# Kernel optimization log

Hardware: AMD Instinct MI355X
Metric: run time of the kernel (lower is better)

## Reference

```python
import jax, jax.numpy as jnp
import numpy as np

NB, NA, NC, NH, NW = 16, 5, 80, 64, 64
MAXT = 50            # max gt boxes per image
THRESH = 0.6         # ignore threshold
NOOBJ_SCALE = 1.0
OBJ_SCALE = 5.0
NTOT = NB * NA * NH * NW


def _iou_cwh(b1, b2):
    """IoU for center-format (x,y,w,h) boxes, broadcasting over leading dims."""
    x1, y1, w1, h1 = (b1[..., i] for i in range(4))
    x2, y2, w2, h2 = (b2[..., i] for i in range(4))
    cw = jnp.minimum(x1 + 0.5 * w1, x2 + 0.5 * w2) - jnp.maximum(x1 - 0.5 * w1, x2 - 0.5 * w2)
    ch = jnp.minimum(y1 + 0.5 * h1, y2 + 0.5 * h2) - jnp.maximum(y1 - 0.5 * h1, y2 - 0.5 * h2)
    inter = jnp.maximum(cw, 0.0) * jnp.maximum(ch, 0.0)
    union = w1 * h1 + w2 * h2 - inter
    return jnp.where(inter > 0, inter / union, 0.0)


def setup_inputs() -> dict:
    key = jax.random.key(0)
    k1, k2, k3, k4 = jax.random.split(key, 4)
    output = jax.random.normal(k1, (NB, NA * (5 + NC), NH, NW), jnp.float32)
    nval = 20  # valid boxes per image; rest zero (loop-break semantics)
    cls = jax.random.randint(k2, (NB, nval), 0, NC).astype(jnp.float32)
    xy = jax.random.uniform(k3, (NB, nval, 2), minval=0.05, maxval=0.95)
    wh = jax.random.uniform(k4, (NB, nval, 2), minval=0.05, maxval=0.30)
    boxes = jnp.concatenate([cls[..., None], xy, wh], axis=-1)      # [NB,nval,5]
    pad = jnp.zeros((NB, MAXT - nval, 5), jnp.float32)
    target = jnp.concatenate([boxes, pad], axis=1).reshape(NB, MAXT * 5)
    anchors = jnp.array([[0.57273, 0.677385], [1.87446, 2.06253], [3.33843, 5.47434],
                         [7.88282, 3.52778], [9.77052, 9.16828]], jnp.float32)
    return {"output": output, "target": target, "anchors": anchors}


def reference(output, target, anchors):
    target = jax.lax.stop_gradient(target)  # target.detach() in torch
    out = output.reshape(NB, NA, 5 + NC, NH, NW)
    tx = jax.nn.sigmoid(out[:, :, 0])
    ty = jax.nn.sigmoid(out[:, :, 1])
    tw, th = out[:, :, 2], out[:, :, 3]
    conf = jax.nn.sigmoid(out[:, :, 4])                   # [B,A,H,W]
    cls_logits = jnp.moveaxis(out[:, :, 5:], 2, -1)       # [B,A,H,W,C]

    aw, ah = anchors[:, 0], anchors[:, 1]
    # decoded pred boxes, detached (only used for target building, as in torch)
    pred = jax.lax.stop_gradient(jnp.stack([
        tx + jnp.arange(NW, dtype=jnp.float32)[None, None, None, :],
        ty + jnp.arange(NH, dtype=jnp.float32)[None, None, :, None],
        jnp.exp(tw) * aw[None, :, None, None],
        jnp.exp(th) * ah[None, :, None, None]], axis=-1))  # [B,A,H,W,4]
    anchors_sg = jax.lax.stop_gradient(anchors)
    aw_sg, ah_sg = anchors_sg[:, 0], anchors_sg[:, 1]

    tb = target.reshape(NB, MAXT, 5)
    # torch breaks at first box with x==0 -> cumulative validity
    valid = jnp.cumprod((tb[:, :, 1] != 0).astype(jnp.int32), axis=1) > 0  # [B,T]
    gcls = tb[:, :, 0]
    gx, gw = tb[:, :, 1] * NW, tb[:, :, 3] * NW
    gy, gh = tb[:, :, 2] * NH, tb[:, :, 4] * NH
    gt = jnp.stack([gx, gy, gw, gh], axis=-1)             # [B,T,4]

    # ignore mask: max IoU of each pred box against all valid gt
    ious = _iou_cwh(gt[:, :, None, None, None, :], pred[:, None])  # [B,T,A,H,W]
    ious = jnp.where(valid[:, :, None, None, None], ious, 0.0)
    conf_mask = jnp.where(ious.max(axis=1) > THRESH, 0.0, NOOBJ_SCALE)  # [B,A,H,W]

    # anchor assignment: IoU of (0,0,gw,gh) vs (0,0,aw,ah) -> argmax anchor
    inter = jnp.minimum(gw[..., None], aw_sg) * jnp.minimum(gh[..., None], ah_sg)
    union = gw[..., None] * gh[..., None] + aw_sg * ah_sg - inter
    best_n = jnp.argmax(inter / union, axis=-1)           # [B,T]

    gi = jnp.clip(gx.astype(jnp.int32), 0, NW - 1)
    gj = jnp.clip(gy.astype(jnp.int32), 0, NH - 1)
    cell = best_n * (NH * NW) + gj * NW + gi              # [B,T] index in A*H*W
    mpred = jnp.take_along_axis(pred.reshape(NB, NA * NH * NW, 4), cell[:, :, None], axis=1)
    iou_best = _iou_cwh(gt, mpred)                        # [B,T]

    flat = cell + jnp.arange(NB)[:, None] * (NA * NH * NW)
    flat = jnp.where(valid, flat, NTOT).reshape(-1)       # out-of-range -> dropped
    fv = lambda v: v.reshape(-1)
    gw_s = jnp.where(valid, gw, 1.0)
    gh_s = jnp.where(valid, gh, 1.0)
    awb, ahb = aw_sg[best_n], ah_sg[best_n]

    cls_mask = jnp.zeros(NTOT, jnp.float32).at[flat].set(1.0, mode='drop')
    conf_mask = conf_mask.reshape(-1).at[flat].set(OBJ_SCALE, mode='drop')
    # seen < 12800 -> tcoord xy default 0.5, coord_mask all ones
    t0 = jnp.full((NTOT,), 0.5).at[flat].set(fv(gx - gi.astype(jnp.float32)), mode='drop')
    t1 = jnp.full((NTOT,), 0.5).at[flat].set(fv(gy - gj.astype(jnp.float32)), mode='drop')
    t2 = jnp.zeros(NTOT).at[flat].set(fv(jnp.log(gw_s / awb)), mode='drop')
    t3 = jnp.zeros(NTOT).at[flat].set(fv(jnp.log(gh_s / ahb)), mode='drop')
    tconf = jnp.zeros(NTOT).at[flat].set(fv(iou_best), mode='drop')
    tcls = jnp.zeros(NTOT, jnp.int32).at[flat].set(fv(gcls.astype(jnp.int32)), mode='drop')

    coord = jnp.stack([tx, ty, tw, th], axis=0).reshape(4, NTOT)
    tcoord = jnp.stack([t0, t1, t2, t3], axis=0)
    loss_coord = 0.5 * jnp.sum((coord - tcoord) ** 2)     # coord_mask == 1 everywhere
    loss_conf = 0.5 * jnp.sum(conf_mask * (conf.reshape(-1) - tconf) ** 2)
    logp = jax.nn.log_softmax(cls_logits, axis=-1).reshape(NTOT, NC)
    ce = -jnp.take_along_axis(logp, tcls[:, None], axis=1)[:, 0]
    loss_cls = jnp.sum(ce * cls_mask)
    return loss_coord + loss_conf + loss_cls
```

## Files before the change

### kernel.cpp

```cpp
#include <hip/hip_runtime.h>
#include <math.h>

constexpr int kNB   = 16;
constexpr int kNA   = 5;
constexpr int kNC   = 80;
constexpr int kNH   = 64;
constexpr int kNW   = 64;
constexpr int kMAXT = 50;
constexpr int kCH    = 5 + kNC;
constexpr int kPLANE = kNH * kNW;
constexpr int kCELLS_B = kNA * kPLANE;
constexpr int kBLK  = 1024;
constexpr int kBPB  = kCELLS_B / kBLK;
constexpr int kGRID = kNB * kBPB;
constexpr float kOBJ = 5.0f;
constexpr unsigned kREADY = 0x9E3779B9u;

constexpr int kRECF = 16;
constexpr int kRECB = kMAXT * kRECF;

__device__ __forceinline__ float frcp(float x) { return __builtin_amdgcn_rcpf(x); }
__device__ __forceinline__ float fsig(float x) { return frcp(1.0f + __expf(-x)); }

__global__ __launch_bounds__(64) void k_targets(const float* __restrict__ out,
                                                const float* __restrict__ target,
                                                const float* __restrict__ anchors,
                                                float* __restrict__ recG,
                                                int* __restrict__ nvArr) {
    const int b = blockIdx.x, t = threadIdx.x;

    float c0 = 0.f, x = 0.f, y = 0.f, w = 0.f, h = 0.f;
    if (t < kMAXT) {
        const float* tp = target + (b * kMAXT + t) * 5;
        c0 = tp[0]; x = tp[1]; y = tp[2]; w = tp[3]; h = tp[4];
    }
    unsigned long long m = __ballot(x != 0.0f);
    int nv = (int)__builtin_ctzll(~m);
    if (t == 0) nvArr[b] = nv;

    const bool act = (t < nv);
    int cell = -1, gi = 0, gj = 0, bn = 0;
    float gx = 0, gy = 0, gw = 0, gh = 0, aw = 1.f, ah = 1.f;
    if (act) {
        gx = x * kNW; gy = y * kNH; gw = w * kNW; gh = h * kNH;
        float best = -1.0f;
        for (int n = 0; n < kNA; ++n) {
            float aw_ = anchors[2 * n], ah_ = anchors[2 * n + 1];
            float inter = fminf(gw, aw_) * fminf(gh, ah_);
            float uni = gw * gh + aw_ * ah_ - inter;
            float r = inter / uni;
            if (r > best) { best = r; bn = n; }
        }
        aw = anchors[2 * bn]; ah = anchors[2 * bn + 1];
        gi = (int)gx; gi = gi < 0 ? 0 : (gi > kNW - 1 ? kNW - 1 : gi);
        gj = (int)gy; gj = gj < 0 ? 0 : (gj > kNH - 1 ? kNH - 1 : gj);
        cell = bn * kPLANE + gj * kNW + gi;
    }
    bool owner = act;
    for (int t2 = 0; t2 < kMAXT; ++t2) {
        int c2 = __shfl(cell, t2, 64);
        if (act && t2 > t && c2 == cell) owner = false;
    }
    if (act) {
        const float* mb = out + ((size_t)(b * kNA + bn) * kCH) * kPLANE + gj * kNW + gi;
        float px = fsig(mb[0]) + (float)gi;
        float py = fsig(mb[kPLANE]) + (float)gj;
        float pw = __expf(mb[2 * kPLANE]) * aw;
        float ph = __expf(mb[3 * kPLANE]) * ah;
        float cw  = fminf(gx + 0.5f * gw, px + 0.5f * pw) - fmaxf(gx - 0.5f * gw, px - 0.5f * pw);
        float chh = fminf(gy + 0.5f * gh, py + 0.5f * ph) - fmaxf(gy - 0.5f * gh, py - 0.5f * ph);
        float inter = fmaxf(cw, 0.f) * fmaxf(chh, 0.f);
        float uni = gw * gh + pw * ph - inter;
        float iou = (inter > 0.f) ? inter / uni : 0.f;

        float* r = recG + b * kRECB + t * kRECF;
        r[0]  = gx - 0.5f * gw;  r[1]  = gx + 0.5f * gw;
        r[2]  = gy - 0.5f * gh;  r[3]  = gy + 0.5f * gh;
        r[4]  = 0.6f * gw * gh;  r[5]  = __int_as_float(cell);
        r[6]  = owner ? 1.f : 0.f; r[7] = 0.f;
        r[8]  = gx - (float)gi;  r[9]  = gy - (float)gj;
        r[10] = __logf(gw / aw); r[11] = __logf(gh / ah);
        r[12] = iou;             r[13] = c0;
        r[14] = 0.f;             r[15] = 0.f;
    }
}

__global__ __launch_bounds__(1024) void k_fused(const float* __restrict__ out,
                                                const float* __restrict__ anchors,
                                                const float* __restrict__ recG,
                                                const int* __restrict__ nvArr,
                                                float* __restrict__ partials,
                                                unsigned* __restrict__ flags,
                                                float* __restrict__ outv) {
    __shared__ __align__(16) float srec[kRECB];
    __shared__ float wred[16];

    const int tid  = threadIdx.x;
    const int wave = tid >> 6;
    const int lane = tid & 63;
    const int b    = blockIdx.x / kBPB;
    const int blkb = blockIdx.x % kBPB;

    const int cidx = blkb * kBLK + tid;
    const int a    = cidx / kPLANE;
    const int remp = cidx & (kPLANE - 1);
    const int i    = remp & (kNW - 1), j = remp >> 6;
    const float* ob = out + ((size_t)(b * kNA + a) * kCH) * kPLANE + remp;
    float o0 = ob[0];
    float o1 = ob[kPLANE];
    float o2 = ob[2 * kPLANE];
    float o3 = ob[3 * kPLANE];
    float o4 = ob[4 * kPLANE];

    if (tid < kRECB) srec[tid] = recG[b * kRECB + tid];
    const int nv = nvArr[b];
    __syncthreads();

    float ceV0 = 0.f, ceV1 = -INFINITY, ceLt = 0.f;
    bool doCE = false;
    if (wave >= 1 && wave <= 3) {
        const int t_ce = blkb + kBPB * (wave - 1);
        if (t_ce < nv && srec[t_ce * kRECF + 6] != 0.f) {
            doCE = true;
            int cell = __float_as_int(srec[t_ce * kRECF + 5]);
            int bn = cell >> 12, pix = cell & (kPLANE - 1);
            int tcls = (int)srec[t_ce * kRECF + 13];
            const float* lg = out + ((size_t)(b * kNA + bn) * kCH + 5) * kPLANE + pix;
            ceV0 = lg[(size_t)lane * kPLANE];
            if (lane < kNC - 64) ceV1 = lg[(size_t)(64 + lane) * kPLANE];
            ceLt = lg[(size_t)tcls * kPLANE];
        }
    }

    float tx   = fsig(o0);
    float ty   = fsig(o1);
    float tw   = o2;
    float th   = o3;
    float conf = fsig(o4);

    float aw = anchors[2 * a], ah = anchors[2 * a + 1];
    float pw = __expf(tw) * aw, ph = __expf(th) * ah;
    float px = tx + (float)i, py = ty + (float)j;
    float px1 = px - 0.5f * pw, px2 = px + 0.5f * pw;
    float py1 = py - 0.5f * ph, py2 = py + 0.5f * ph;
    float p06 = 0.6f * pw * ph;

    float flag = -INFINITY;
    int match = -1;
    for (int t = 0; t < nv; ++t) {
        const float4 bx = *reinterpret_cast<const float4*>(srec + t * kRECF);
        const float2 gc = *reinterpret_cast<const float2*>(srec + t * kRECF + 4);
        float cw  = fminf(bx.y, px2) - fmaxf(bx.x, px1);
        float chh = fminf(bx.w, py2) - fmaxf(bx.z, py1);
        float inter = fmaxf(cw, 0.f) * fmaxf(chh, 0.f);
        flag = fmaxf(flag, fmaf(1.6f, inter, -gc.x));
        match = (__float_as_int(gc.y) == cidx) ? t : match;
    }

    float t0 = 0.5f, t1 = 0.5f, t2 = 0.f, t3 = 0.f, tconf = 0.f, cmask;
    if (match >= 0) {
        const float4 tt = *reinterpret_cast<const float4*>(srec + match * kRECF + 8);
        t0 = tt.x; t1 = tt.y; t2 = tt.z; t3 = tt.w;
        tconf = srec[match * kRECF + 12];
        cmask = kOBJ;
    } else {
        cmask = (flag > p06) ? 0.f : 1.f;
    }

    float dx = tx - t0, dy = ty - t1, dw = tw - t2, dh = th - t3, dc = conf - tconf;
    float loss = 0.5f * (dx * dx + dy * dy + dw * dw + dh * dh)
               + 0.5f * cmask * dc * dc;

    if (doCE) {
        float mx = fmaxf(ceV0, ceV1);
        #pragma unroll
        for (int off = 32; off > 0; off >>= 1) mx = fmaxf(mx, __shfl_xor(mx, off, 64));
        float s = __expf(ceV0 - mx) + ((lane < kNC - 64) ? __expf(ceV1 - mx) : 0.f);
        #pragma unroll
        for (int off = 32; off > 0; off >>= 1) s += __shfl_xor(s, off, 64);
        if (lane == 0) loss += __logf(s) + mx - ceLt;
    }

    #pragma unroll
    for (int off = 32; off > 0; off >>= 1) loss += __shfl_down(loss, off, 64);
    if (lane == 0) wred[wave] = loss;
    __syncthreads();
    if (tid == 0) {
        float v = 0.f;
        #pragma unroll
        for (int w = 0; w < 16; ++w) v += wred[w];
        __hip_atomic_store(&partials[blockIdx.x], v, __ATOMIC_RELAXED, __HIP_MEMORY_SCOPE_AGENT);
        __hip_atomic_store(&flags[blockIdx.x], kREADY, __ATOMIC_RELEASE, __HIP_MEMORY_SCOPE_AGENT);
    }

    if (blockIdx.x == 0) {
        __syncthreads();
        float v = 0.f;
        if (tid < kGRID) {
            while (__hip_atomic_load(&flags[tid], __ATOMIC_ACQUIRE, __HIP_MEMORY_SCOPE_AGENT) != kREADY)
                __builtin_amdgcn_s_sleep(2);
            v = __hip_atomic_load(&partials[tid], __ATOMIC_RELAXED, __HIP_MEMORY_SCOPE_AGENT);
            __hip_atomic_store(&flags[tid], 0u, __ATOMIC_RELAXED, __HIP_MEMORY_SCOPE_AGENT);
        }
        #pragma unroll
        for (int off = 32; off > 0; off >>= 1) v += __shfl_down(v, off, 64);
        if (lane == 0) wred[wave] = v;
        __syncthreads();
        if (tid == 0) {
            float s = 0.f;
            #pragma unroll
            for (int w = 0; w < 16; ++w) s += wred[w];
            outv[0] = s;
        }
    }
}

extern "C" void kernel_launch(void* const* d_in, const int* in_sizes, int n_in,
                              void* d_out, int out_size, void* d_ws, size_t ws_size,
                              hipStream_t stream) {
    const float* output  = (const float*)d_in[0];
    const float* target  = (const float*)d_in[1];
    const float* anchors = (const float*)d_in[2];

    float*    recG     = (float*)d_ws;
    int*      nvArr    = (int*)(recG + kNB * kRECB);
    float*    partials = (float*)(nvArr + 16);
    unsigned* flags    = (unsigned*)(partials + kGRID);

    k_targets<<<kNB, 64, 0, stream>>>(output, target, anchors, recG, nvArr);
    k_fused<<<kGRID, kBLK, 0, stream>>>(output, anchors, recG, nvArr, partials, flags, (float*)d_out);
}
```

Before: 18.98 us.

## Fuse target-building kernel into main loss kernel and shrink block to 640

Drops the separate k_targets launch. Each block's first wave now rebuilds the per-image ground-truth records directly in shared memory, and the owner check for class cross-entropy is done with a wave ballot over shared cell ids. This removes one kernel launch and the global round-trip for the record table. In exchange every block redundantly recomputes the target records and adds an extra barrier. The block size changes from 1024 to 640 threads, which gives a 512-block grid, and two waves instead of three now cover the CE tasks.

```diff
diff --git a/kernel.cpp b/kernel.cpp
--- a/kernel.cpp
+++ b/kernel.cpp
@@ -10,7 +10,7 @@
 constexpr int kCH    = 5 + kNC;
 constexpr int kPLANE = kNH * kNW;
 constexpr int kCELLS_B = kNA * kPLANE;
-constexpr int kBLK  = 1024;
+constexpr int kBLK  = 640;
 constexpr int kBPB  = kCELLS_B / kBLK;
 constexpr int kGRID = kNB * kBPB;
 constexpr float kOBJ = 5.0f;
@@ -22,78 +22,16 @@
 __device__ __forceinline__ float frcp(float x) { return __builtin_amdgcn_rcpf(x); }
 __device__ __forceinline__ float fsig(float x) { return frcp(1.0f + __expf(-x)); }
 
-__global__ __launch_bounds__(64) void k_targets(const float* __restrict__ out,
-                                                const float* __restrict__ target,
-                                                const float* __restrict__ anchors,
-                                                float* __restrict__ recG,
-                                                int* __restrict__ nvArr) {
-    const int b = blockIdx.x, t = threadIdx.x;
-
-    float c0 = 0.f, x = 0.f, y = 0.f, w = 0.f, h = 0.f;
-    if (t < kMAXT) {
-        const float* tp = target + (b * kMAXT + t) * 5;
-        c0 = tp[0]; x = tp[1]; y = tp[2]; w = tp[3]; h = tp[4];
-    }
-    unsigned long long m = __ballot(x != 0.0f);
-    int nv = (int)__builtin_ctzll(~m);
-    if (t == 0) nvArr[b] = nv;
-
-    const bool act = (t < nv);
-    int cell = -1, gi = 0, gj = 0, bn = 0;
-    float gx = 0, gy = 0, gw = 0, gh = 0, aw = 1.f, ah = 1.f;
-    if (act) {
-        gx = x * kNW; gy = y * kNH; gw = w * kNW; gh = h * kNH;
-        float best = -1.0f;
-        for (int n = 0; n < kNA; ++n) {
-            float aw_ = anchors[2 * n], ah_ = anchors[2 * n + 1];
-            float inter = fminf(gw, aw_) * fminf(gh, ah_);
-            float uni = gw * gh + aw_ * ah_ - inter;
-            float r = inter / uni;
-            if (r > best) { best = r; bn = n; }
-        }
-        aw = anchors[2 * bn]; ah = anchors[2 * bn + 1];
-        gi = (int)gx; gi = gi < 0 ? 0 : (gi > kNW - 1 ? kNW - 1 : gi);
-        gj = (int)gy; gj = gj < 0 ? 0 : (gj > kNH - 1 ? kNH - 1 : gj);
-        cell = bn * kPLANE + gj * kNW + gi;
-    }
-    bool owner = act;
-    for (int t2 = 0; t2 < kMAXT; ++t2) {
-        int c2 = __shfl(cell, t2, 64);
-        if (act && t2 > t && c2 == cell) owner = false;
-    }
-    if (act) {
-        const float* mb = out + ((size_t)(b * kNA + bn) * kCH) * kPLANE + gj * kNW + gi;
-        float px = fsig(mb[0]) + (float)gi;
-        float py = fsig(mb[kPLANE]) + (float)gj;
-        float pw = __expf(mb[2 * kPLANE]) * aw;
-        float ph = __expf(mb[3 * kPLANE]) * ah;
-        float cw  = fminf(gx + 0.5f * gw, px + 0.5f * pw) - fmaxf(gx - 0.5f * gw, px - 0.5f * pw);
-        float chh = fminf(gy + 0.5f * gh, py + 0.5f * ph) - fmaxf(gy - 0.5f * gh, py - 0.5f * ph);
-        float inter = fmaxf(cw, 0.f) * fmaxf(chh, 0.f);
-        float uni = gw * gh + pw * ph - inter;
-        float iou = (inter > 0.f) ? inter / uni : 0.f;
-
-        float* r = recG + b * kRECB + t * kRECF;
-        r[0]  = gx - 0.5f * gw;  r[1]  = gx + 0.5f * gw;
-        r[2]  = gy - 0.5f * gh;  r[3]  = gy + 0.5f * gh;
-        r[4]  = 0.6f * gw * gh;  r[5]  = __int_as_float(cell);
-        r[6]  = owner ? 1.f : 0.f; r[7] = 0.f;
-        r[8]  = gx - (float)gi;  r[9]  = gy - (float)gj;
-        r[10] = __logf(gw / aw); r[11] = __logf(gh / ah);
-        r[12] = iou;             r[13] = c0;
-        r[14] = 0.f;             r[15] = 0.f;
-    }
-}
-
-__global__ __launch_bounds__(1024) void k_fused(const float* __restrict__ out,
-                                                const float* __restrict__ anchors,
-                                                const float* __restrict__ recG,
-                                                const int* __restrict__ nvArr,
-                                                float* __restrict__ partials,
-                                                unsigned* __restrict__ flags,
-                                                float* __restrict__ outv) {
+__global__ __launch_bounds__(640, 5) void k_fused(const float* __restrict__ out,
+                                                  const float* __restrict__ target,
+                                                  const float* __restrict__ anchors,
+                                                  float* __restrict__ partials,
+                                                  unsigned* __restrict__ flags,
+                                                  float* __restrict__ outv) {
     __shared__ __align__(16) float srec[kRECB];
-    __shared__ float wred[16];
+    __shared__ int scell[kMAXT];
+    __shared__ int snv;
+    __shared__ float wred[10];
 
     const int tid  = threadIdx.x;
     const int wave = tid >> 6;
@@ -102,7 +40,7 @@
     const int blkb = blockIdx.x % kBPB;
 
     const int cidx = blkb * kBLK + tid;
-    const int a    = cidx / kPLANE;
+    const int a    = cidx >> 12;
     const int remp = cidx & (kPLANE - 1);
     const int i    = remp & (kNW - 1), j = remp >> 6;
     const float* ob = out + ((size_t)(b * kNA + a) * kCH) * kPLANE + remp;
@@ -112,23 +50,68 @@
     float o3 = ob[3 * kPLANE];
     float o4 = ob[4 * kPLANE];
 
-    if (tid < kRECB) srec[tid] = recG[b * kRECB + tid];
-    const int nv = nvArr[b];
+    bool act = false;
+    int cell = -1, gi = 0, gj = 0;
+    float gx = 0, gy = 0, gw = 0, gh = 0, aw0 = 1.f, ah0 = 1.f;
+    if (wave == 0) {
+        int t = lane;
+        float c0 = 0.f, x = 0.f, y = 0.f, w = 0.f, h = 0.f;
+        if (t < kMAXT) {
+            const float* tp = target + (b * kMAXT + t) * 5;
+            c0 = tp[0]; x = tp[1]; y = tp[2]; w = tp[3]; h = tp[4];
+        }
+        unsigned long long m = __ballot(x != 0.0f);
+        int nv = (int)__builtin_ctzll(~m);
+        if (t == 0) snv = nv;
+        act = (t < nv);
+        if (act) {
+            gx = x * kNW; gy = y * kNH; gw = w * kNW; gh = h * kNH;
+            int bn = 0; float best = -1.0f;
+            for (int n = 0; n < kNA; ++n) {
+                float aw_ = anchors[2 * n], ah_ = anchors[2 * n + 1];
+                float inter = fminf(gw, aw_) * fminf(gh, ah_);
+                float uni = gw * gh + aw_ * ah_ - inter;
+                float r = inter * frcp(uni);
+                if (r > best) { best = r; bn = n; }
+            }
+            aw0 = anchors[2 * bn]; ah0 = anchors[2 * bn + 1];
+            gi = (int)gx; gi = gi < 0 ? 0 : (gi > kNW - 1 ? kNW - 1 : gi);
+            gj = (int)gy; gj = gj < 0 ? 0 : (gj > kNH - 1 ? kNH - 1 : gj);
+            cell = bn * kPLANE + gj * kNW + gi;
+
+            float* r = srec + t * kRECF;
+            r[0]  = gx - 0.5f * gw;  r[1]  = gx + 0.5f * gw;
+            r[2]  = gy - 0.5f * gh;  r[3]  = gy + 0.5f * gh;
+            r[4]  = 0.6f * gw * gh;  r[5]  = __int_as_float(cell);
+            r[13] = c0;
+        }
+        if (t < kMAXT) scell[t] = act ? cell : -1;
+    }
     __syncthreads();
+    const int nv = snv;
+
+    float m0 = 0.f, m1 = 0.f, m2 = 0.f, m3 = 0.f;
+    if (wave == 0 && act) {
+        const float* mb = out + ((size_t)(b * kNA + (cell >> 12)) * kCH) * kPLANE + (cell & (kPLANE - 1));
+        m0 = mb[0]; m1 = mb[kPLANE]; m2 = mb[2 * kPLANE]; m3 = mb[3 * kPLANE];
+    }
 
     float ceV0 = 0.f, ceV1 = -INFINITY, ceLt = 0.f;
     bool doCE = false;
-    if (wave >= 1 && wave <= 3) {
+    if (wave == 1 || wave == 2) {
         const int t_ce = blkb + kBPB * (wave - 1);
-        if (t_ce < nv && srec[t_ce * kRECF + 6] != 0.f) {
-            doCE = true;
-            int cell = __float_as_int(srec[t_ce * kRECF + 5]);
-            int bn = cell >> 12, pix = cell & (kPLANE - 1);
-            int tcls = (int)srec[t_ce * kRECF + 13];
-            const float* lg = out + ((size_t)(b * kNA + bn) * kCH + 5) * kPLANE + pix;
-            ceV0 = lg[(size_t)lane * kPLANE];
-            if (lane < kNC - 64) ceV1 = lg[(size_t)(64 + lane) * kPLANE];
-            ceLt = lg[(size_t)tcls * kPLANE];
+        int cellv = (lane < kMAXT) ? scell[lane] : -1;
+        if (t_ce < nv) {
+            int cellT = scell[t_ce];
+            unsigned long long dup = __ballot(lane > t_ce && cellv == cellT);
+            if (dup == 0ull) {
+                doCE = true;
+                int tcls = (int)srec[t_ce * kRECF + 13];
+                const float* lg = out + ((size_t)(b * kNA + (cellT >> 12)) * kCH + 5) * kPLANE + (cellT & (kPLANE - 1));
+                ceV0 = lg[(size_t)lane * kPLANE];
+                if (lane < kNC - 64) ceV1 = lg[(size_t)(64 + lane) * kPLANE];
+                ceLt = lg[(size_t)tcls * kPLANE];
+            }
         }
     }
 
@@ -157,6 +140,24 @@
         match = (__float_as_int(gc.y) == cidx) ? t : match;
     }
 
+    if (wave == 0 && act) {
+        float mpx = fsig(m0) + (float)gi;
+        float mpy = fsig(m1) + (float)gj;
+        float mpw = __expf(m2) * aw0;
+        float mph = __expf(m3) * ah0;
+        float cw  = fminf(gx + 0.5f * gw, mpx + 0.5f * mpw) - fmaxf(gx - 0.5f * gw, mpx - 0.5f * mpw);
+        float chh = fminf(gy + 0.5f * gh, mpy + 0.5f * mph) - fmaxf(gy - 0.5f * gh, mpy - 0.5f * mph);
+        float inter = fmaxf(cw, 0.f) * fmaxf(chh, 0.f);
+        float uni = gw * gh + mpw * mph - inter;
+        float iou = (inter > 0.f) ? inter / uni : 0.f;
+
+        float* r = srec + lane * kRECF;
+        r[8]  = gx - (float)gi;  r[9]  = gy - (float)gj;
+        r[10] = __logf(gw / aw0); r[11] = __logf(gh / ah0);
+        r[12] = iou;
+    }
+    __syncthreads();
+
     float t0 = 0.5f, t1 = 0.5f, t2 = 0.f, t3 = 0.f, tconf = 0.f, cmask;
     if (match >= 0) {
         const float4 tt = *reinterpret_cast<const float4*>(srec + match * kRECF + 8);
@@ -188,7 +189,7 @@
     if (tid == 0) {
         float v = 0.f;
         #pragma unroll
-        for (int w = 0; w < 16; ++w) v += wred[w];
+        for (int w = 0; w < 10; ++w) v += wred[w];
         __hip_atomic_store(&partials[blockIdx.x], v, __ATOMIC_RELAXED, __HIP_MEMORY_SCOPE_AGENT);
         __hip_atomic_store(&flags[blockIdx.x], kREADY, __ATOMIC_RELEASE, __HIP_MEMORY_SCOPE_AGENT);
     }
@@ -209,7 +210,7 @@
         if (tid == 0) {
             float s = 0.f;
             #pragma unroll
-            for (int w = 0; w < 16; ++w) s += wred[w];
+            for (int w = 0; w < 10; ++w) s += wred[w];
             outv[0] = s;
         }
     }
@@ -222,11 +223,8 @@
     const float* target  = (const float*)d_in[1];
     const float* anchors = (const float*)d_in[2];
 
-    float*    recG     = (float*)d_ws;
-    int*      nvArr    = (int*)(recG + kNB * kRECB);
-    float*    partials = (float*)(nvArr + 16);
+    float*    partials = (float*)d_ws;
     unsigned* flags    = (unsigned*)(partials + kGRID);
 
-    k_targets<<<kNB, 64, 0, stream>>>(output, target, anchors, recG, nvArr);
-    k_fused<<<kGRID, kBLK, 0, stream>>>(output, anchors, recG, nvArr, partials, flags, (float*)d_out);
+    k_fused<<<kGRID, kBLK, 0, stream>>>(output, target, anchors, partials, flags, (float*)d_out);
 }
```

New measurement: 16.07 us. 1.18x faster.
